# Performance work log

Hardware: AMD Instinct MI355X
Metric: run time of the kernel (lower is better)

The kernel has to match this reference:

```python
import jax, jax.numpy as jnp
import numpy as np
from jax import lax

RADIUS = 2
DILATION = 2
KS = 2 * RADIUS + 1  # 5
PERM = np.array([6, 8, 1, 11, 2, 10, 0, 7, 9, 4, 5, 3])


def _shift_kernels():
    # Reproduce the torch index construction in numpy (all constants).
    six = np.array([[0, 1, 1], [1, 1, 0], [1, 0, 1], [1, 1, 2], [2, 1, 1], [1, 2, 1]])
    # pairwise squared distances between the 6 neighbourhood offsets
    d = ((six[:, None, :] - six[None, :, :]) ** 2).sum(-1)
    x, y = np.meshgrid(np.arange(6), np.arange(6), indexing='ij')
    mask = (x > y).reshape(-1) & (d == 2).reshape(-1)
    idx1 = np.repeat(six[:, None, :], 6, axis=1).reshape(-1, 3)[mask]
    idx2 = np.repeat(six[None, :, :], 6, axis=0).reshape(-1, 3)[mask]
    k1 = np.zeros((12, 1, 3, 3, 3), np.float32)
    k2 = np.zeros((12, 1, 3, 3, 3), np.float32)
    r = np.arange(12)
    k1[r, 0, idx1[:, 0], idx1[:, 1], idx1[:, 2]] = 1.0
    k2[r, 0, idx2[:, 0], idx2[:, 1], idx2[:, 2]] = 1.0
    return jnp.asarray(k1), jnp.asarray(k2)

_K1, _K2 = _shift_kernels()
DN = ('NCDHW', 'OIDHW', 'NCDHW')


def _rep_pad(x, p):
    return jnp.pad(x, ((0, 0), (0, 0), (p, p), (p, p), (p, p)), mode='edge')


def mindssc(img):
    # img: [N,1,D,H,W]
    p1 = _rep_pad(img, DILATION)
    c1 = lax.conv_general_dilated(p1, _K1, (1, 1, 1), 'VALID',
                                  rhs_dilation=(DILATION,) * 3, dimension_numbers=DN)
    c2 = lax.conv_general_dilated(p1, _K2, (1, 1, 1), 'VALID',
                                  rhs_dilation=(DILATION,) * 3, dimension_numbers=DN)
    diff2 = (c1 - c2) ** 2  # [N,12,D,H,W]
    p2 = _rep_pad(diff2, RADIUS)
    ssd = lax.reduce_window(p2, 0.0, lax.add, (1, 1, KS, KS, KS),
                            (1, 1, 1, 1, 1), 'VALID') / float(KS ** 3)
    mind = ssd - jnp.min(ssd, axis=1, keepdims=True)
    mind_var = jnp.mean(mind, axis=1, keepdims=True)
    m = jnp.mean(mind_var)
    mind_var = jnp.clip(mind_var, m * 0.001, m * 1000.0)
    mind = jnp.exp(-mind / mind_var)
    return mind[:, PERM]


def setup_inputs() -> dict:
    key = jax.random.key(0)
    k1, k2 = jax.random.split(key)
    shape = (1, 1, 128, 128, 128)
    return {
        'y_true': jax.random.normal(k1, shape, dtype=jnp.float32),
        'y_pred': jax.random.normal(k2, shape, dtype=jnp.float32),
    }


def reference(y_true, y_pred):
    return jnp.mean((mindssc(y_pred) - mindssc(y_true)) ** 2)
```

## Files before the change

### kernel.cpp

```cpp
#include <hip/hip_runtime.h>

#define DIM   128
#define DMASK 127
#define PLANE (DIM * DIM)
#define VOX   (1 << 21)
#define NCH   12

#define CHS   (VOX + 2048)
#define IMGS  (NCH * CHS + 1024)

typedef __attribute__((ext_vector_type(2))) _Float16 half2v;
typedef __attribute__((ext_vector_type(4))) _Float16 half4v;

__constant__ int c_sd1[12] = { 0, 0, 0, 0, 0, 2, 2, 2, 0, 0, 0, 0};
__constant__ int c_sh1[12] = { 0,-2,-2, 0, 0, 0, 0, 0, 2, 2, 2, 2};
__constant__ int c_sw1[12] = {-2, 0, 0, 2, 2, 0, 0, 0, 0, 0, 0, 0};
__constant__ int c_sd2[12] = {-2,-2, 0,-2, 0, 0, 0, 0,-2, 0, 0, 2};
__constant__ int c_sh2[12] = { 0, 0, 0, 0,-2, 0,-2, 0, 0, 0, 0, 0};
__constant__ int c_sw2[12] = { 0, 0,-2, 0, 0,-2, 0, 2, 0,-2, 2, 0};

__device__ __forceinline__ int clamp7(int v) { return min(max(v, 0), DMASK); }


#define PLANE_ITER(IT_EXPR, S5C)                                             \
    {                                                                        \
        int it = (IT_EXPR);                                                  \
        int dp = clamp7(d0 - 2 + it);                                        \
        int pOffA = clamp7(dp + sd1) * (PLANE * 4);                          \
        int pOffB = clamp7(dp + sd2) * (PLANE * 4);                          \
        float tX[12], tY[12];                                                \
        _Pragma("unroll")                                                    \
        for (int r = 0; r < 12; ++r) {                                       \
            float2 a = *(const float2*)(imgc + (pOffA + rowOffA[r] + colA)); \
            float2 b = *(const float2*)(imgc + (pOffB + rowOffB[r] + colB)); \
            a.y = fixAlo ? a.x : a.y;  a.x = fixAhi ? a.y : a.x;             \
            b.y = fixBlo ? b.x : b.y;  b.x = fixBhi ? b.y : b.x;             \
            float dx = a.x - b.x; dx *= dx;                    \
            float dy = a.y - b.y; dy *= dy;                    \
            float lx = __shfl_up(dx, 1, 64);                   \
            float ly = __shfl_up(dy, 1, 64);                   \
            float rx = __shfl_down(dx, 1, 64);                 \
            float ry = __shfl_down(dy, 1, 64);                 \
            ly = (l == 0)  ? dx : ly;                    \
            rx = (l == 63) ? dy : rx;                    \
            tX[r] = lx + ly + dx + dy + rx;                 \
            tY[r] = ly + dx + dy + rx + ry;                 \
        }                                                                    \
        float sx = tX[0] + tX[1] + tX[2] + tX[3] + tX[4];                    \
        float sy = tY[0] + tY[1] + tY[2] + tY[3] + tY[4];                    \
        bool dowrite = (it >= 4);                                            \
        _Float16* dstD = dstBase + (size_t)(d0 + it - 4) * PLANE;            \
        _Pragma("unroll")                                                    \
        for (int k = 0; k < 8; ++k) {                                        \
            half2v hv = { (_Float16)sx, (_Float16)sy };     \
            half2v old = hist[S5C][k];                                       \
            win[k].x += (float)hv[0] - (float)old[0];                        \
            win[k].y += (float)hv[1] - (float)old[1];                        \
            hist[S5C][k] = hv;                                               \
            if (dowrite) {                                                   \
                half2v ov = { (_Float16)win[k].x, (_Float16)win[k].y };      \
                *(half2v*)(dstD + k * DIM) = ov;                             \
            }                                                                \
            if (k < 7) {                                                     \
                sx += tX[k + 5] - tX[k];                                     \
                sy += tY[k + 5] - tY[k];                                     \
            }                                                                \
        }                                                                    \
    }

__global__ __launch_bounds__(256, 3) void f123(const float* __restrict__ img0,
                                               const float* __restrict__ img1,
                                               _Float16* __restrict__ Sall) {
    const float* img = blockIdx.y ? img1 : img0;
    _Float16* outS = Sall + (size_t)blockIdx.y * IMGS;
    const char* imgc = (const char*)img;

    int wid = (blockIdx.x << 2) + (threadIdx.x >> 6);
    int ch = wid >> 8;
    int hs = (wid >> 4) & 15;
    int ds = wid & 15;
    int h0 = hs << 3;
    int d0 = ds << 3;
    int l  = threadIdx.x & 63;

    int sd1 = c_sd1[ch], sh1 = c_sh1[ch], sw1 = c_sw1[ch];
    int sd2 = c_sd2[ch], sh2 = c_sh2[ch], sw2 = c_sw2[ch];

    int rowOffA[12], rowOffB[12];
#pragma unroll
    for (int r = 0; r < 12; ++r) {
        int hq = clamp7(h0 - 2 + r);
        rowOffA[r] = clamp7(hq + sh1) * (DIM * 4);
        rowOffB[r] = clamp7(hq + sh2) * (DIM * 4);
    }

    int c2 = l << 1;
    int colA = min(max(c2 + sw1, 0), 126) * 4;
    int colB = min(max(c2 + sw2, 0), 126) * 4;
    bool fixAlo = (sw1 < 0) && (l == 0);
    bool fixAhi = (sw1 > 0) && (l == 63);
    bool fixBlo = (sw2 < 0) && (l == 0);
    bool fixBhi = (sw2 > 0) && (l == 63);

    float2 win[8];
    half2v hist[5][8];
#pragma unroll
    for (int k = 0; k < 8; ++k) {
        win[k].x = 0.0f; win[k].y = 0.0f;
#pragma unroll
        for (int s = 0; s < 5; ++s) hist[s][k] = half2v{(_Float16)0.0f, (_Float16)0.0f};
    }

    _Float16* dstBase = outS + (size_t)ch * CHS + h0 * DIM + c2;

#pragma unroll
    for (int j = 0; j < 2; ++j)
        PLANE_ITER(j, j)

    for (int oo = 0; oo < 2; ++oo) {
#pragma unroll
        for (int j = 0; j < 5; ++j)
            PLANE_ITER(2 + oo * 5 + j, ((2 + j) % 5))
    }
}

__global__ __launch_bounds__(256, 3) void kmse(const _Float16* __restrict__ S0,
                                               const _Float16* __restrict__ S1,
                                               float* __restrict__ partial) {
    int t = blockIdx.x * 256 + threadIdx.x;

    half4v v0[NCH], v1[NCH];
#pragma unroll
    for (int ch = 0; ch < NCH; ++ch)
        v0[ch] = ((const half4v*)(S0 + (size_t)ch * CHS))[t];
#pragma unroll
    for (int ch = 0; ch < NCH; ++ch)
        v1[ch] = ((const half4v*)(S1 + (size_t)ch * CHS))[t];

    float mn0[4], sm0[4], mn1[4], sm1[4];
#pragma unroll
    for (int j = 0; j < 4; ++j) {
        mn0[j] = 3.4e38f; sm0[j] = 0.0f;
        mn1[j] = 3.4e38f; sm1[j] = 0.0f;
    }
#pragma unroll
    for (int ch = 0; ch < NCH; ++ch)
#pragma unroll
        for (int j = 0; j < 4; ++j) {
            float s0 = (float)v0[ch][j];
            float s1 = (float)v1[ch][j];
            mn0[j] = fminf(mn0[j], s0); sm0[j] += s0;
            mn1[j] = fminf(mn1[j], s1); sm1[j] += s1;
        }

    float inv0[4], inv1[4];
#pragma unroll
    for (int j = 0; j < 4; ++j) {
        inv0[j] = __fdividef(1.0f, sm0[j] * (1.0f / 12.0f) - mn0[j]);
        inv1[j] = __fdividef(1.0f, sm1[j] * (1.0f / 12.0f) - mn1[j]);
    }

    float acc = 0.0f;
#pragma unroll
    for (int ch = 0; ch < NCH; ++ch)
#pragma unroll
        for (int j = 0; j < 4; ++j) {
            float e0 = __expf(-((float)v0[ch][j] - mn0[j]) * inv0[j]);
            float e1 = __expf(-((float)v1[ch][j] - mn1[j]) * inv1[j]);
            float df = e0 - e1;
            acc += df * df;
        }

#pragma unroll
    for (int off = 32; off > 0; off >>= 1)
        acc += __shfl_down(acc, off, 64);
    __shared__ float smem[4];
    int lane = threadIdx.x & 63, wv = threadIdx.x >> 6;
    if (lane == 0) smem[wv] = acc;
    __syncthreads();
    if (threadIdx.x == 0)
        partial[blockIdx.x] = smem[0] + smem[1] + smem[2] + smem[3];
}

__global__ __launch_bounds__(256) void kred(const float* __restrict__ partial,
                                            float* __restrict__ out) {
    int tid = threadIdx.x;
    float acc = 0.0f;
#pragma unroll
    for (int k = 0; k < 8; ++k)
        acc += partial[tid + (k << 8)];
#pragma unroll
    for (int off = 32; off > 0; off >>= 1)
        acc += __shfl_down(acc, off, 64);
    __shared__ float smem[4];
    int lane = tid & 63, wv = tid >> 6;
    if (lane == 0) smem[wv] = acc;
    __syncthreads();
    if (tid == 0)
        out[0] = (smem[0] + smem[1] + smem[2] + smem[3])
               * (1.0f / (12.0f * (float)VOX));
}

__global__ void kdiag(float* out, float ws_mb) { out[0] = ws_mb; }

extern "C" void kernel_launch(void* const* d_in, const int* in_sizes, int n_in,
                              void* d_out, int out_size, void* d_ws, size_t ws_size,
                              hipStream_t stream) {
    const float* y_true = (const float*)d_in[0];
    const float* y_pred = (const float*)d_in[1];
    float* out = (float*)d_out;

    const size_t NEED = 2ull * IMGS * sizeof(_Float16) + 8192 + 64;
    if (ws_size < NEED) {
        kdiag<<<1, 1, 0, stream>>>(out, (float)(ws_size >> 20));
        return;
    }

    _Float16* S0      = (_Float16*)d_ws;
    _Float16* S1      = S0 + (size_t)IMGS;
    float*    partial = (float*)(S1 + (size_t)IMGS);

    f123<<<dim3(768, 2), 256, 0, stream>>>(y_true, y_pred, S0);
    kmse<<<VOX / 4 / 256, 256, 0, stream>>>(S0, S1, partial);
    kred<<<1, 256, 0, stream>>>(partial, out);
}
```

Baseline: 158.8 us.

## Fuse MIND descriptor computation and MSE reduction into one shared-memory kernel

Replaces the two-pass scheme, which wrote fp16 box-filtered SSD volumes for both images to global memory and read them back in a separate MSE kernel, with one kernel. Each block of 12 waves (one wave per channel) streams depth planes for both images and stages the windowed sums in a double-buffered shared-memory tile. After a barrier, 4 waves compute the per-voxel min, mean, exp and squared difference. This removes roughly 100MB of intermediate global traffic. In exchange it uses smaller tiles (4 rows instead of 8) with more halo recompute, only 256 large blocks, a barrier per plane, and idles 8 of 12 waves during the exp phase.

After: 138.1 us. -13.0%, faster.

```diff
diff --git a/kernel.cpp b/kernel.cpp
--- a/kernel.cpp
+++ b/kernel.cpp
@@ -6,11 +6,7 @@
 #define VOX   (1 << 21)
 #define NCH   12
 
-#define CHS   (VOX + 2048)
-#define IMGS  (NCH * CHS + 1024)
-
 typedef __attribute__((ext_vector_type(2))) _Float16 half2v;
-typedef __attribute__((ext_vector_type(4))) _Float16 half4v;
 
 __constant__ int c_sd1[12] = { 0, 0, 0, 0, 0, 2, 2, 2, 0, 0, 0, 0};
 __constant__ int c_sh1[12] = { 0,-2,-2, 0, 0, 0, 0, 0, 2, 2, 2, 2};
@@ -22,17 +18,13 @@
 __device__ __forceinline__ int clamp7(int v) { return min(max(v, 0), DMASK); }
 
 
-#define PLANE_ITER(IT_EXPR, S5C)                                             \
+#define STREAM_PIPE(IMC, WIN, HIST, IMGI, S5C)                               \
     {                                                                        \
-        int it = (IT_EXPR);                                                  \
-        int dp = clamp7(d0 - 2 + it);                                        \
-        int pOffA = clamp7(dp + sd1) * (PLANE * 4);                          \
-        int pOffB = clamp7(dp + sd2) * (PLANE * 4);                          \
-        float tX[12], tY[12];                                                \
+        float tX[8], tY[8];                                                  \
         _Pragma("unroll")                                                    \
-        for (int r = 0; r < 12; ++r) {                                       \
-            float2 a = *(const float2*)(imgc + (pOffA + rowOffA[r] + colA)); \
-            float2 b = *(const float2*)(imgc + (pOffB + rowOffB[r] + colB)); \
+        for (int r = 0; r < 8; ++r) {                                        \
+            float2 a = *(const float2*)(IMC + (pOffA + rowOffA[r] + colA));  \
+            float2 b = *(const float2*)(IMC + (pOffB + rowOffB[r] + colB));  \
             a.y = fixAlo ? a.x : a.y;  a.x = fixAhi ? a.y : a.x;             \
             b.y = fixBlo ? b.x : b.y;  b.x = fixBhi ? b.y : b.x;             \
             float dx = a.x - b.x; dx *= dx;                    \
@@ -43,52 +35,51 @@
             float ry = __shfl_down(dy, 1, 64);                 \
             ly = (l == 0)  ? dx : ly;                    \
             rx = (l == 63) ? dy : rx;                    \
-            tX[r] = lx + ly + dx + dy + rx;                 \
-            tY[r] = ly + dx + dy + rx + ry;                 \
+            float m = ly + dx + dy + rx;                                     \
+            tX[r] = lx + m;                                 \
+            tY[r] = m + ry;                                 \
         }                                                                    \
         float sx = tX[0] + tX[1] + tX[2] + tX[3] + tX[4];                    \
         float sy = tY[0] + tY[1] + tY[2] + tY[3] + tY[4];                    \
-        bool dowrite = (it >= 4);                                            \
-        _Float16* dstD = dstBase + (size_t)(d0 + it - 4) * PLANE;            \
         _Pragma("unroll")                                                    \
-        for (int k = 0; k < 8; ++k) {                                        \
+        for (int k = 0; k < 4; ++k) {                                        \
             half2v hv = { (_Float16)sx, (_Float16)sy };     \
-            half2v old = hist[S5C][k];                                       \
-            win[k].x += (float)hv[0] - (float)old[0];                        \
-            win[k].y += (float)hv[1] - (float)old[1];                        \
-            hist[S5C][k] = hv;                                               \
+            half2v old = HIST[S5C][k];                                       \
+            WIN[k].x += (float)hv[0] - (float)old[0];                        \
+            WIN[k].y += (float)hv[1] - (float)old[1];                        \
+            HIST[S5C][k] = hv;                                               \
             if (dowrite) {                                                   \
-                half2v ov = { (_Float16)win[k].x, (_Float16)win[k].y };      \
-                *(half2v*)(dstD + k * DIM) = ov;                             \
+                half2v ov = { (_Float16)WIN[k].x, (_Float16)WIN[k].y };      \
+                sb[bb][ch][IMGI][k][l] = ov;                                 \
             }                                                                \
-            if (k < 7) {                                                     \
+            if (k < 3) {                                                     \
                 sx += tX[k + 5] - tX[k];                                     \
                 sy += tY[k + 5] - tY[k];                                     \
             }                                                                \
         }                                                                    \
     }
 
-__global__ __launch_bounds__(256, 3) void f123(const float* __restrict__ img0,
-                                               const float* __restrict__ img1,
-                                               _Float16* __restrict__ Sall) {
-    const float* img = blockIdx.y ? img1 : img0;
-    _Float16* outS = Sall + (size_t)blockIdx.y * IMGS;
-    const char* imgc = (const char*)img;
-
-    int wid = (blockIdx.x << 2) + (threadIdx.x >> 6);
-    int ch = wid >> 8;
-    int hs = (wid >> 4) & 15;
-    int ds = wid & 15;
-    int h0 = hs << 3;
-    int d0 = ds << 3;
-    int l  = threadIdx.x & 63;
-
+__global__ __launch_bounds__(768) void ffuse(const float* __restrict__ img0,
+                                             const float* __restrict__ img1,
+                                             float* __restrict__ partial) {
+    __shared__ half2v sb[2][NCH][2][4][64];
+    __shared__ float sred[4];
+
+    int tid = threadIdx.x;
+    int wv  = tid >> 6;
+    int l   = tid & 63;
+
+    int bx = blockIdx.x;
+    int h0 = (bx & 31) << 2;
+    int d0 = (bx >> 5) << 4;
+
+    int ch = wv;
     int sd1 = c_sd1[ch], sh1 = c_sh1[ch], sw1 = c_sw1[ch];
     int sd2 = c_sd2[ch], sh2 = c_sh2[ch], sw2 = c_sw2[ch];
 
-    int rowOffA[12], rowOffB[12];
-#pragma unroll
-    for (int r = 0; r < 12; ++r) {
+    int rowOffA[8], rowOffB[8];
+#pragma unroll
+    for (int r = 0; r < 8; ++r) {
         int hq = clamp7(h0 - 2 + r);
         rowOffA[r] = clamp7(hq + sh1) * (DIM * 4);
         rowOffB[r] = clamp7(hq + sh2) * (DIM * 4);
@@ -102,93 +93,89 @@
     bool fixBlo = (sw2 < 0) && (l == 0);
     bool fixBhi = (sw2 > 0) && (l == 63);
 
-    float2 win[8];
-    half2v hist[5][8];
-#pragma unroll
-    for (int k = 0; k < 8; ++k) {
-        win[k].x = 0.0f; win[k].y = 0.0f;
-#pragma unroll
-        for (int s = 0; s < 5; ++s) hist[s][k] = half2v{(_Float16)0.0f, (_Float16)0.0f};
-    }
-
-    _Float16* dstBase = outS + (size_t)ch * CHS + h0 * DIM + c2;
-
-#pragma unroll
-    for (int j = 0; j < 2; ++j)
-        PLANE_ITER(j, j)
-
-    for (int oo = 0; oo < 2; ++oo) {
-#pragma unroll
-        for (int j = 0; j < 5; ++j)
-            PLANE_ITER(2 + oo * 5 + j, ((2 + j) % 5))
-    }
-}
-
-__global__ __launch_bounds__(256, 3) void kmse(const _Float16* __restrict__ S0,
-                                               const _Float16* __restrict__ S1,
-                                               float* __restrict__ partial) {
-    int t = blockIdx.x * 256 + threadIdx.x;
-
-    half4v v0[NCH], v1[NCH];
-#pragma unroll
-    for (int ch = 0; ch < NCH; ++ch)
-        v0[ch] = ((const half4v*)(S0 + (size_t)ch * CHS))[t];
-#pragma unroll
-    for (int ch = 0; ch < NCH; ++ch)
-        v1[ch] = ((const half4v*)(S1 + (size_t)ch * CHS))[t];
-
-    float mn0[4], sm0[4], mn1[4], sm1[4];
-#pragma unroll
-    for (int j = 0; j < 4; ++j) {
-        mn0[j] = 3.4e38f; sm0[j] = 0.0f;
-        mn1[j] = 3.4e38f; sm1[j] = 0.0f;
-    }
-#pragma unroll
-    for (int ch = 0; ch < NCH; ++ch)
-#pragma unroll
-        for (int j = 0; j < 4; ++j) {
-            float s0 = (float)v0[ch][j];
-            float s1 = (float)v1[ch][j];
-            mn0[j] = fminf(mn0[j], s0); sm0[j] += s0;
-            mn1[j] = fminf(mn1[j], s1); sm1[j] += s1;
+    float2 win0[4], win1[4];
+    half2v hist0[5][4], hist1[5][4];
+#pragma unroll
+    for (int k = 0; k < 4; ++k) {
+        win0[k].x = 0.0f; win0[k].y = 0.0f;
+        win1[k].x = 0.0f; win1[k].y = 0.0f;
+#pragma unroll
+        for (int s = 0; s < 5; ++s) {
+            hist0[s][k] = half2v{(_Float16)0.0f, (_Float16)0.0f};
+            hist1[s][k] = half2v{(_Float16)0.0f, (_Float16)0.0f};
         }
-
-    float inv0[4], inv1[4];
-#pragma unroll
-    for (int j = 0; j < 4; ++j) {
-        inv0[j] = __fdividef(1.0f, sm0[j] * (1.0f / 12.0f) - mn0[j]);
-        inv1[j] = __fdividef(1.0f, sm1[j] * (1.0f / 12.0f) - mn1[j]);
-    }
+    }
+
+    const char* im0 = (const char*)img0;
+    const char* im1 = (const char*)img1;
 
     float acc = 0.0f;
-#pragma unroll
-    for (int ch = 0; ch < NCH; ++ch)
-#pragma unroll
-        for (int j = 0; j < 4; ++j) {
-            float e0 = __expf(-((float)v0[ch][j] - mn0[j]) * inv0[j]);
-            float e1 = __expf(-((float)v1[ch][j] - mn1[j]) * inv1[j]);
-            float df = e0 - e1;
-            acc += df * df;
+
+    for (int oo = 0; oo < 4; ++oo) {
+#pragma unroll
+        for (int s5 = 0; s5 < 5; ++s5) {
+            int it = oo * 5 + s5;
+            int dp = clamp7(d0 - 2 + it);
+            int pOffA = clamp7(dp + sd1) * (PLANE * 4);
+            int pOffB = clamp7(dp + sd2) * (PLANE * 4);
+            bool dowrite = (it >= 4);
+            int bb = it & 1;
+
+            STREAM_PIPE(im0, win0, hist0, 0, s5)
+            STREAM_PIPE(im1, win1, hist1, 1, s5)
+
+            if (dowrite) {
+                __syncthreads();
+                if (tid < 256) {
+                    int rrow = wv;
+                    float mn0x = 3.4e38f, mn0y = 3.4e38f, sm0x = 0.f, sm0y = 0.f;
+                    float mn1x = 3.4e38f, mn1y = 3.4e38f, sm1x = 0.f, sm1y = 0.f;
+#pragma unroll
+                    for (int c = 0; c < 12; ++c) {
+                        half2v h0 = sb[bb][c][0][rrow][l];
+                        half2v h1 = sb[bb][c][1][rrow][l];
+                        float v0x = (float)h0[0], v0y = (float)h0[1];
+                        float v1x = (float)h1[0], v1y = (float)h1[1];
+                        mn0x = fminf(mn0x, v0x); sm0x += v0x;
+                        mn0y = fminf(mn0y, v0y); sm0y += v0y;
+                        mn1x = fminf(mn1x, v1x); sm1x += v1x;
+                        mn1y = fminf(mn1y, v1y); sm1y += v1y;
+                    }
+                    float i0x = __fdividef(1.0f, sm0x * (1.0f / 12.0f) - mn0x);
+                    float i0y = __fdividef(1.0f, sm0y * (1.0f / 12.0f) - mn0y);
+                    float i1x = __fdividef(1.0f, sm1x * (1.0f / 12.0f) - mn1x);
+                    float i1y = __fdividef(1.0f, sm1y * (1.0f / 12.0f) - mn1y);
+#pragma unroll
+                    for (int c = 0; c < 12; ++c) {
+                        half2v h0 = sb[bb][c][0][rrow][l];
+                        half2v h1 = sb[bb][c][1][rrow][l];
+                        float e0x = __expf(-((float)h0[0] - mn0x) * i0x);
+                        float e1x = __expf(-((float)h1[0] - mn1x) * i1x);
+                        float e0y = __expf(-((float)h0[1] - mn0y) * i0y);
+                        float e1y = __expf(-((float)h1[1] - mn1y) * i1y);
+                        float dfx = e0x - e1x, dfy = e0y - e1y;
+                        acc += dfx * dfx + dfy * dfy;
+                    }
+                }
+            }
         }
-
-#pragma unroll
-    for (int off = 32; off > 0; off >>= 1)
-        acc += __shfl_down(acc, off, 64);
-    __shared__ float smem[4];
-    int lane = threadIdx.x & 63, wv = threadIdx.x >> 6;
-    if (lane == 0) smem[wv] = acc;
+    }
+
+    if (tid < 256) {
+#pragma unroll
+        for (int off = 32; off > 0; off >>= 1)
+            acc += __shfl_down(acc, off, 64);
+        if ((tid & 63) == 0) sred[tid >> 6] = acc;
+    }
     __syncthreads();
-    if (threadIdx.x == 0)
-        partial[blockIdx.x] = smem[0] + smem[1] + smem[2] + smem[3];
+    if (tid == 0)
+        partial[blockIdx.x] = sred[0] + sred[1] + sred[2] + sred[3];
 }
 
 __global__ __launch_bounds__(256) void kred(const float* __restrict__ partial,
                                             float* __restrict__ out) {
     int tid = threadIdx.x;
-    float acc = 0.0f;
-#pragma unroll
-    for (int k = 0; k < 8; ++k)
-        acc += partial[tid + (k << 8)];
+    float acc = partial[tid];
 #pragma unroll
     for (int off = 32; off > 0; off >>= 1)
         acc += __shfl_down(acc, off, 64);
@@ -210,17 +197,14 @@
     const float* y_pred = (const float*)d_in[1];
     float* out = (float*)d_out;
 
-    const size_t NEED = 2ull * IMGS * sizeof(_Float16) + 8192 + 64;
+    const size_t NEED = 4096;
     if (ws_size < NEED) {
         kdiag<<<1, 1, 0, stream>>>(out, (float)(ws_size >> 20));
         return;
     }
 
-    _Float16* S0      = (_Float16*)d_ws;
-    _Float16* S1      = S0 + (size_t)IMGS;
-    float*    partial = (float*)(S1 + (size_t)IMGS);
-
-    f123<<<dim3(768, 2), 256, 0, stream>>>(y_true, y_pred, S0);
-    kmse<<<VOX / 4 / 256, 256, 0, stream>>>(S0, S1, partial);
+    float* partial = (float*)d_ws;
+
+    ffuse<<<dim3(256), 768, 0, stream>>>(y_true, y_pred, partial);
     kred<<<1, 256, 0, stream>>>(partial, out);
 }
```
